# Optimization experiments

Measured on AMD Instinct MI355X. Metric: run time of the kernel, lower is better.

The kernel has to match this reference:

```python
import jax, jax.numpy as jnp
import numpy as np
from jax import lax

N_CLASS = 21
K_ED = 5
ALPHA = 0.1
BN_EPS = 1e-5


def _conv(x, w):
    # NCHW conv, stride 1, SAME padding
    return lax.conv_general_dilated(x, w, (1, 1), 'SAME',
                                    dimension_numbers=('NCHW', 'OIHW', 'NCHW'))


def _bn(x, g, b, m, v):
    # inference-mode BatchNorm2d with running stats
    scale = (g * lax.rsqrt(v + BN_EPS))[None, :, None, None]
    return (x - m[None, :, None, None]) * scale + b[None, :, None, None]


def _maxpool(x, k):
    return lax.reduce_window(x, -jnp.inf, lax.max, (1, 1, k, k), (1, 1, 1, 1), 'SAME')


def setup_inputs() -> dict:
    key = jax.random.key(0)
    ks = jax.random.split(key, 12)
    N, F, H, W, C = 8, 512, 96, 96, N_CLASS
    feature = jax.random.normal(ks[0], (N, F, H, W), jnp.float32)
    global_pred = jax.random.normal(ks[1], (N, C, H, W), jnp.float32)
    conv1_w = jax.random.normal(ks[2], (256, F, 3, 3), jnp.float32) * 0.02
    bn1_g = jnp.ones((256,), jnp.float32)
    bn1_b = jnp.zeros((256,), jnp.float32)
    bn1_m = jax.random.normal(ks[3], (256,), jnp.float32) * 0.1
    bn1_v = jax.random.uniform(ks[4], (256,), jnp.float32, 0.5, 1.5)
    conv2_w = jax.random.normal(ks[5], (128, 256, 3, 3), jnp.float32) * 0.02
    bn2_g = jnp.ones((128,), jnp.float32)
    bn2_b = jnp.zeros((128,), jnp.float32)
    bn2_m = jax.random.normal(ks[6], (128,), jnp.float32) * 0.1
    bn2_v = jax.random.uniform(ks[7], (128,), jnp.float32, 0.5, 1.5)
    conv3_w = jax.random.normal(ks[8], (C, 128, 1, 1), jnp.float32) * 0.02
    conv3_b = jnp.zeros((C,), jnp.float32)
    return dict(feature=feature, global_pred=global_pred,
                conv1_w=conv1_w, bn1_g=bn1_g, bn1_b=bn1_b, bn1_m=bn1_m, bn1_v=bn1_v,
                conv2_w=conv2_w, bn2_g=bn2_g, bn2_b=bn2_b, bn2_m=bn2_m, bn2_v=bn2_v,
                conv3_w=conv3_w, conv3_b=conv3_b)


def reference(feature, global_pred, conv1_w, bn1_g, bn1_b, bn1_m, bn1_v,
              conv2_w, bn2_g, bn2_b, bn2_m, bn2_v, conv3_w, conv3_b):
    N, F, H, W = feature.shape
    # hard labels -> one-hot [N, C, H, W]
    lbl = jnp.argmax(global_pred, axis=1)
    onehot = jnp.transpose(jax.nn.one_hot(lbl, N_CLASS, dtype=feature.dtype), (0, 3, 1, 2))
    # binary morphology: dilation = max-pool, erosion = -max-pool(-x)
    d = _maxpool(onehot, K_ED)
    e = -_maxpool(-onehot, K_ED)
    transition = jnp.sum(d - e, axis=1, keepdims=True)
    transition = jnp.where(transition >= 1.0, 1.0, transition)  # [N,1,H,W]
    tfeat = feature * transition
    # per-class masked mean over ALL H*W pixels (faithful to .mean(dim=2))
    objs = jnp.einsum('nfhw,nchw->ncf', feature, e) / (H * W)  # [N,C,F]
    # cdist(p=2) between transition-feature pixels and class prototypes
    x = tfeat.reshape(N, F, H * W).transpose(0, 2, 1)  # [N,HW,F]
    x2 = jnp.sum(x * x, axis=-1, keepdims=True)
    o2 = jnp.sum(objs * objs, axis=-1)
    d2 = jnp.maximum(x2 + o2[:, None, :] - 2.0 * jnp.einsum('npf,ncf->npc', x, objs), 0.0)
    cd = jnp.where(d2 > 0, jnp.sqrt(jnp.where(d2 > 0, d2, 1.0)), 0.0)  # safe sqrt
    dist = 1.0 - jax.nn.softmax(cd, axis=-1)  # [N,HW,C]
    obj_feat = jnp.einsum('npc,ncf->nfp', dist, objs).reshape(N, F, H, W)
    fusion = (feature * (1.0 - transition)
              + feature * transition * ALPHA
              + obj_feat * transition * (1.0 - ALPHA))
    # fusion_predictor: convBNReLU -> bilinear x2 -> convBNReLU -> 1x1 conv
    h = jax.nn.relu(_bn(_conv(fusion, conv1_w), bn1_g, bn1_b, bn1_m, bn1_v))
    h = jax.image.resize(h, (N, 256, 2 * H, 2 * W), method='bilinear')
    h = jax.nn.relu(_bn(_conv(h, conv2_w), bn2_g, bn2_b, bn2_m, bn2_v))
    logits = _conv(h, conv3_w) + conv3_b[None, :, None, None]
    # eval mode: softmax over classes
    return jax.nn.softmax(logits, axis=1)
```

## Files before the change

kernel.cpp:

```cpp
#include <hip/hip_runtime.h>
#include <cstdint>
#include <cstddef>

typedef __attribute__((ext_vector_type(4))) float f32x4;
typedef __attribute__((ext_vector_type(8))) short short8;

__device__ __forceinline__ float bf2f(unsigned short u) {
  union { unsigned int i; float f; } x; x.i = ((unsigned int)u) << 16; return x.f;
}
__device__ __forceinline__ unsigned short f2bf(float f) {
  union { float f; unsigned int i; } x; x.f = f;
  unsigned int r = x.i + 0x7fffu + ((x.i >> 16) & 1u);
  return (unsigned short)(r >> 16);
}
__device__ __forceinline__ void gload16(unsigned short* lds, const unsigned short* g) {
  __builtin_amdgcn_global_load_lds(
      (const __attribute__((address_space(1))) unsigned int*)g,
      (__attribute__((address_space(3))) unsigned int*)lds, 16, 0, 0);
}

__global__ void k_prepbn(const float* __restrict__ g1, const float* __restrict__ b1,
                         const float* __restrict__ m1, const float* __restrict__ v1,
                         const float* __restrict__ g2, const float* __restrict__ b2,
                         const float* __restrict__ m2, const float* __restrict__ v2,
                         float* __restrict__ s1, float* __restrict__ bb1,
                         float* __restrict__ s2, float* __restrict__ bb2) {
  int i = threadIdx.x;
  if (i < 256) { float s = g1[i] * rsqrtf(v1[i] + 1e-5f); s1[i] = s; bb1[i] = b1[i] - m1[i] * s; }
  if (i < 128) { float s = g2[i] * rsqrtf(v2[i] + 1e-5f); s2[i] = s; bb2[i] = b2[i] - m2[i] * s; }
}

__global__ void k_prepw1(const float* __restrict__ w, unsigned short* __restrict__ wt) {
  int i = blockIdx.x * 256 + threadIdx.x;
  int o = i / 4608, k = i - o * 4608;
  int cblk = k / 288, r = k - cblk * 288;
  int t = r >> 5, cl = r & 31;
  int ci = cblk * 32 + cl;
  int ty = t / 3, tx = t - ty * 3;
  wt[i] = f2bf(w[((o * 512 + ci) * 3 + ty) * 3 + tx]);
}
__global__ void k_prepw2(const float* __restrict__ w, unsigned short* __restrict__ wt) {
  int i = blockIdx.x * 256 + threadIdx.x;
  int o = i / 2304, k = i - o * 2304;
  int cblk = k / 288, r = k - cblk * 288;
  int t = r >> 5, cl = r & 31;
  int ci = cblk * 32 + cl;
  int ty = t / 3, tx = t - ty * 3;
  wt[i] = f2bf(w[((o * 256 + ci) * 3 + ty) * 3 + tx]);
}
__global__ void k_prepw3(const float* __restrict__ w3, unsigned short* __restrict__ w3b) {
  int i = blockIdx.x * 256 + threadIdx.x;
  int c = i >> 7, k = i & 127;
  w3b[i] = (c < 21) ? f2bf(w3[c * 128 + k]) : (unsigned short)0;
}

template <int HP, int WP, int C>
__global__ void k_border(unsigned short* __restrict__ p) {
  const int B = 2 * WP + 2 * (HP - 2);
  const int total = 8 * B * (C / 8);
  int i = blockIdx.x * 256 + threadIdx.x;
  if (i >= total) return;
  const int cg = i % (C / 8);
  int b = i / (C / 8);
  const int n = b / B; b -= n * B;
  int y, x;
  if (b < WP) { y = 0; x = b; }
  else if (b < 2 * WP) { y = HP - 1; x = b - WP; }
  else { int r = b - 2 * WP; y = 1 + (r >> 1); x = (r & 1) ? (WP - 1) : 0; }
  short8 z = {0, 0, 0, 0, 0, 0, 0, 0};
  *(short8*)&p[(((long)n * HP + y) * WP + x) * C + cg * 8] = z;
}

__global__ __launch_bounds__(256)
void k_featT(const float* __restrict__ feat, unsigned short* __restrict__ featT) {
  const int g = blockIdx.x * 256 + threadIdx.x;
  const int n = g / 9216, p = g - n * 9216;
  const int fg0 = blockIdx.y * 16;
  const float* src = feat + (long)n * 512 * 9216 + p;
  unsigned short* dst = featT + ((long)n * 9216 + p) * 512;
  for (int fg = fg0; fg < fg0 + 16; fg++) {
    short8 o;
    #pragma unroll
    for (int j = 0; j < 8; j++) o[j] = (short)f2bf(src[(long)(fg * 8 + j) * 9216]);
    *(short8*)&dst[fg * 8] = o;
  }
}

__global__ void k_labels(const float* __restrict__ gp, signed char* __restrict__ lab) {
  int p = blockIdx.x * 256 + threadIdx.x;
  int n = p / 9216, q = p - n * 9216;
  const float* g = gp + (long)n * 21 * 9216 + q;
  float best = g[0]; int bi = 0;
  #pragma unroll
  for (int c = 1; c < 21; c++) {
    float v = g[(long)c * 9216];
    if (v > best) { best = v; bi = c; }
  }
  lab[p] = (signed char)bi;
}

__global__ void k_em(const signed char* __restrict__ lab, signed char* __restrict__ em) {
  int p = blockIdx.x * 256 + threadIdx.x;
  int n = p / 9216, q = p - n * 9216, y = q / 96, x = q - y * 96;
  const signed char* L = lab + n * 9216;
  signed char l0 = L[q];
  bool uni = true;
  for (int dy = -2; dy <= 2; dy++) {
    int yy = y + dy; if (yy < 0 || yy > 95) continue;
    for (int dx = -2; dx <= 2; dx++) {
      int xx = x + dx; if (xx < 0 || xx > 95) continue;
      uni = uni && (L[yy * 96 + xx] == l0);
    }
  }
  em[p] = uni ? l0 : (signed char)-1;
}

__global__ __launch_bounds__(256)
void k_objsT(const unsigned short* __restrict__ featT, const signed char* __restrict__ em,
             float* __restrict__ objs) {
  __shared__ float part[21 * 512];
  __shared__ signed char emL[256];
  __shared__ int pres[21];
  const int b = blockIdx.x;
  const int n = b / 36;
  const int px0 = (b - n * 36) * 256;
  const int tid = threadIdx.x;
  for (int i = tid; i < 21 * 512; i += 256) part[i] = 0.f;
  if (tid < 21) pres[tid] = 0;
  emL[tid] = em[n * 9216 + px0 + tid];
  __syncthreads();
  const unsigned short* base = featT + ((long)n * 9216 + px0) * 512 + tid * 2;
  for (int px = 0; px < 256; px++) {
    const int c0 = emL[px];
    if (c0 >= 0) {
      if (tid == 0) pres[c0] = 1;
      unsigned int v = *(const unsigned int*)&base[(long)px * 512];
      atomicAdd(&part[c0 * 512 + tid * 2], bf2f((unsigned short)(v & 0xffff)));
      atomicAdd(&part[c0 * 512 + tid * 2 + 1], bf2f((unsigned short)(v >> 16)));
    }
  }
  __syncthreads();
  for (int i = tid; i < 21 * 512; i += 256) {
    const int c = i >> 9;
    if (pres[c]) atomicAdd(&objs[(long)n * 21 * 512 + i], part[i] * (1.0f / 9216.0f));
  }
}

__global__ void k_o2(const float* __restrict__ objs, float* __restrict__ o2) {
  int nc = blockIdx.x;
  int lane = threadIdx.x;
  const float* o = objs + (long)nc * 512;
  float s = 0.f;
  for (int f = lane; f < 512; f += 64) { float v = o[f]; s += v * v; }
  #pragma unroll
  for (int off = 32; off; off >>= 1) s += __shfl_down(s, off);
  if (lane == 0) o2[nc] = s;
}

__global__ void k_objsbf(const float* __restrict__ objs, unsigned short* __restrict__ oc) {
  int i = blockIdx.x * 256 + threadIdx.x;
  int n = i / (32 * 512); int r = i - n * 32 * 512;
  int c = r >> 9, f = r & 511;
  oc[i] = (c < 21) ? f2bf(objs[((long)n * 21 + c) * 512 + f]) : (unsigned short)0;
}

__global__ __launch_bounds__(256)
void k_dist_mfma(const unsigned short* __restrict__ featT,
                 const unsigned short* __restrict__ objs_c,
                 const float* __restrict__ o2, float* __restrict__ dist) {
  const int n = blockIdx.y;
  const int w = threadIdx.x >> 6, lane = threadIdx.x & 63;
  const int lrow = lane & 15, kg = lane >> 4;
  const int px = blockIdx.x * 64 + w * 16 + lrow;
  const unsigned short* fb = featT + ((long)n * 9216 + px) * 512 + kg * 8;
  const unsigned short* a0p = objs_c + ((long)n * 32 + lrow) * 512 + kg * 8;
  const unsigned short* a1p = a0p + 16 * 512;
  f32x4 acc0 = {0.f, 0.f, 0.f, 0.f}, acc1 = {0.f, 0.f, 0.f, 0.f};
  float x2 = 0.f;
  #pragma unroll
  for (int s = 0; s < 16; s++) {
    const short8 b = *(const short8*)&fb[s * 32];
    const short8 a0 = *(const short8*)&a0p[s * 32];
    const short8 a1 = *(const short8*)&a1p[s * 32];
    acc0 = __builtin_amdgcn_mfma_f32_16x16x32_bf16(a0, b, acc0, 0, 0, 0);
    acc1 = __builtin_amdgcn_mfma_f32_16x16x32_bf16(a1, b, acc1, 0, 0, 0);
    #pragma unroll
    for (int j = 0; j < 8; j++) { float v = bf2f((unsigned short)b[j]); x2 += v * v; }
  }
  x2 += __shfl_xor(x2, 16); x2 += __shfl_xor(x2, 32);
  float cd[8], mx = -1e30f;
  #pragma unroll
  for (int r = 0; r < 4; r++) {
    const int c = kg * 4 + r;
    float d2 = x2 + o2[n * 21 + c] - 2.f * acc0[r];
    cd[r] = sqrtf(fmaxf(d2, 0.f)); mx = fmaxf(mx, cd[r]);
  }
  #pragma unroll
  for (int r = 0; r < 4; r++) {
    const int c = 16 + kg * 4 + r;
    if (c < 21) {
      float d2 = x2 + o2[n * 21 + c] - 2.f * acc1[r];
      cd[4 + r] = sqrtf(fmaxf(d2, 0.f)); mx = fmaxf(mx, cd[4 + r]);
    } else cd[4 + r] = -1e30f;
  }
  mx = fmaxf(mx, __shfl_xor(mx, 16)); mx = fmaxf(mx, __shfl_xor(mx, 32));
  float sum = 0.f;
  #pragma unroll
  for (int k = 0; k < 8; k++) {
    cd[k] = (cd[k] > -1e29f) ? __expf(cd[k] - mx) : 0.f;
    sum += cd[k];
  }
  sum += __shfl_xor(sum, 16); sum += __shfl_xor(sum, 32);
  const float inv = 1.f / sum;
  #pragma unroll
  for (int r = 0; r < 4; r++)
    dist[((long)n * 21 + kg * 4 + r) * 9216 + px] = 1.f - cd[r] * inv;
  #pragma unroll
  for (int r = 0; r < 4; r++) {
    const int c = 16 + kg * 4 + r;
    if (c < 21) dist[((long)n * 21 + c) * 9216 + px] = 1.f - cd[4 + r] * inv;
  }
}

__global__ __launch_bounds__(256)
void k_fusion(const unsigned short* __restrict__ featT, const signed char* __restrict__ em,
              const float* __restrict__ dist, const float* __restrict__ objs,
              unsigned short* __restrict__ fuP) {
  __shared__ float ob[21 * 512];
  __shared__ float dl[64][21];
  __shared__ signed char eml[64];
  const int blk = blockIdx.x;
  const int n = blk / 144;
  const int p0 = (blk - n * 144) * 64;
  const int tid = threadIdx.x;
  for (int i = tid; i < 21 * 512; i += 256) ob[i] = objs[(long)n * 21 * 512 + i];
  for (int i = tid; i < 64 * 21; i += 256) {
    int px = i & 63, c = i >> 6;
    dl[px][c] = dist[((long)n * 21 + c) * 9216 + p0 + px];
  }
  if (tid < 64) eml[tid] = em[n * 9216 + p0 + tid];
  __syncthreads();
  const int px = tid & 63;
  const int fg = (tid >> 6) * 8;
  const int q = p0 + px;
  const int y = q / 96, x = q - y * 96;
  unsigned short* dst = fuP + (((long)n * 98 + y + 1) * 98 + (x + 1)) * 512;
  const bool t = eml[px] < 0;
  const unsigned short* srcT = featT + ((long)n * 9216 + q) * 512;
  for (int f0 = 0; f0 < 512; f0 += 32) {
    short8 o;
    const short8 fvv = *(const short8*)&srcT[f0 + fg];
    #pragma unroll
    for (int j = 0; j < 8; j++) {
      const int f = f0 + fg + j;
      float fv = bf2f((unsigned short)fvv[j]);
      if (t) {
        float of = 0.f;
        #pragma unroll
        for (int c = 0; c < 21; c++) of += dl[px][c] * ob[c * 512 + f];
        fv = 0.1f * fv + 0.9f * of;
      }
      o[j] = (short)f2bf(fv);
    }
    *(short8*)&dst[fg] = o;
    dst += 32;
  }
}

template <int CIN, int NK>
__global__ __launch_bounds__(256)
void conv3x3_gemm(const unsigned short* __restrict__ inP,
                  const unsigned short* __restrict__ wT,
                  const float* __restrict__ scale, const float* __restrict__ bias,
                  unsigned short* __restrict__ out,
                  int Hout, int Wout, int Hp, int Wp, int COUT, int nbN) {
  __shared__ unsigned short ldsA[4][4096];
  __shared__ unsigned short ldsB[4][4096];
  const int tid = threadIdx.x;
  const int chunk = gridDim.x >> 3;
  const int bid = (blockIdx.x & 7) * chunk + (blockIdx.x >> 3);
  const int mb = bid / nbN, nb = bid - mb * nbN;
  const int bm0 = mb * 128, bn0 = nb * 128;
  const int KT = 9 * CIN;
  const int HWo = Hout * Wout;

  const int rA = tid >> 2;
  const int ch8 = (((tid & 3) ^ ((tid >> 3) & 3)) * 8);
  const int m0 = bm0 + rA, m1 = m0 + 64;
  const int n0 = m0 / HWo; const int q0 = m0 - n0 * HWo;
  const int y0 = q0 / Wout, x0 = q0 - y0 * Wout;
  const int n1 = m1 / HWo; const int q1 = m1 - n1 * HWo;
  const int y1 = q1 / Wout, x1 = q1 - y1 * Wout;
  const unsigned short* gA0 = inP + ((long)(n0 * Hp + y0) * Wp + x0) * CIN + ch8;
  const unsigned short* gA1 = inP + ((long)(n1 * Hp + y1) * Wp + x1) * CIN + ch8;
  const unsigned short* gB0 = wT + (long)(bn0 + rA) * KT + ch8;
  const unsigned short* gB1 = wT + (long)(bn0 + rA + 64) * KT + ch8;

  const int lane = tid & 63;
  const int wv = tid >> 6;
  const int wr = wv >> 1, wc = wv & 1;
  const int lrow = lane & 15, kg = lane >> 4;
  const int arow = wr * 64 + lrow;
  const int aoff = arow * 32 + (kg ^ ((arow >> 1) & 3)) * 8;
  const int brow = wc * 64 + lrow;
  const int boff = brow * 32 + (kg ^ ((brow >> 1) & 3)) * 8;

  f32x4 acc[4][4];
  const f32x4 zero = {0.f, 0.f, 0.f, 0.f};
  #pragma unroll
  for (int i = 0; i < 4; i++)
    #pragma unroll
    for (int j = 0; j < 4; j++) acc[i][j] = zero;

  auto stage = [&](int b, int s) {
    const int cblk = s / 9;
    const int t = s - cblk * 9;
    const int ty = t / 3, tx = t - ty * 3;
    const long offA = (long)(ty * Wp + tx) * CIN + cblk * 32;
    gload16(&ldsA[b][tid * 8], gA0 + offA);
    gload16(&ldsA[b][2048 + tid * 8], gA1 + offA);
    const long k0 = (long)s * 32;
    gload16(&ldsB[b][tid * 8], gB0 + k0);
    gload16(&ldsB[b][2048 + tid * 8], gB1 + k0);
  };

  auto kstep = [&](int rd) {
    const unsigned short* A = ldsA[rd];
    const unsigned short* B = ldsB[rd];
    short8 af[4], bfr[4];
    #pragma unroll
    for (int i = 0; i < 4; i++) af[i] = *(const short8*)&A[aoff + i * 512];
    #pragma unroll
    for (int j = 0; j < 4; j++) bfr[j] = *(const short8*)&B[boff + j * 512];
    __builtin_amdgcn_s_setprio(1);
    #pragma unroll
    for (int i = 0; i < 4; i++)
      #pragma unroll
      for (int j = 0; j < 4; j++)
        acc[i][j] = __builtin_amdgcn_mfma_f32_16x16x32_bf16(af[i], bfr[j], acc[i][j], 0, 0, 0);
    __builtin_amdgcn_s_setprio(0);
  };

  stage(0, 0);
  stage(1, 1);
  stage(2, 2);
  for (int s = 0; s < NK; ++s) {
    if (s <= NK - 3)
      asm volatile("s_waitcnt vmcnt(8)" ::: "memory");
    else if (s == NK - 2)
      asm volatile("s_waitcnt vmcnt(4)" ::: "memory");
    else
      asm volatile("s_waitcnt vmcnt(0)" ::: "memory");
    __builtin_amdgcn_s_barrier();
    asm volatile("" ::: "memory");
    kstep(s & 3);
    if (s + 3 < NK) stage((s + 3) & 3, s + 3);
  }

  #pragma unroll
  for (int i = 0; i < 4; i++) {
    const int row = bm0 + wr * 64 + i * 16 + kg * 4;
    #pragma unroll
    for (int j = 0; j < 4; j++) {
      const int col = bn0 + wc * 64 + j * 16 + lrow;
      const float sc = scale[col], bi = bias[col];
      #pragma unroll
      for (int r = 0; r < 4; r++) {
        float v = acc[i][j][r] * sc + bi;
        v = v > 0.f ? v : 0.f;
        out[(long)(row + r) * COUT + col] = f2bf(v);
      }
    }
  }
}

__global__ __launch_bounds__(256)
void conv2_fused(const unsigned short* __restrict__ inP,
                 const unsigned short* __restrict__ wT,
                 const float* __restrict__ scale, const float* __restrict__ bias,
                 const unsigned short* __restrict__ w3b, const float* __restrict__ b3,
                 float* __restrict__ out) {
  constexpr int CIN = 256, NK = 72;
  constexpr int Wout = 192, Hp = 194, Wp = 194;
  constexpr int HWo = 192 * 192;
  constexpr int KT = 9 * CIN;
  __shared__ unsigned short pool[6 * 4096];
  const int tid = threadIdx.x;
  const int chunk = gridDim.x >> 3;
  const int bid = (blockIdx.x & 7) * chunk + (blockIdx.x >> 3);
  const int bm0 = bid * 128;

  const int rA = tid >> 2;
  const int ch8 = (((tid & 3) ^ ((tid >> 3) & 3)) * 8);
  const int m0 = bm0 + rA, m1 = m0 + 64;
  const int n0 = m0 / HWo; const int q0 = m0 - n0 * HWo;
  const int y0 = q0 / Wout, x0 = q0 - y0 * Wout;
  const int n1 = m1 / HWo; const int q1 = m1 - n1 * HWo;
  const int y1 = q1 / Wout, x1 = q1 - y1 * Wout;
  const unsigned short* gA0 = inP + ((long)(n0 * Hp + y0) * Wp + x0) * CIN + ch8;
  const unsigned short* gA1 = inP + ((long)(n1 * Hp + y1) * Wp + x1) * CIN + ch8;
  const unsigned short* gB0 = wT + (long)rA * KT + ch8;
  const unsigned short* gB1 = wT + (long)(rA + 64) * KT + ch8;

  const int lane = tid & 63;
  const int wv = tid >> 6;
  const int wr = wv >> 1, wc = wv & 1;
  const int lrow = lane & 15, kg = lane >> 4;
  const int arow = wr * 64 + lrow;
  const int aoff = arow * 32 + (kg ^ ((arow >> 1) & 3)) * 8;
  const int brow = wc * 64 + lrow;
  const int boff = brow * 32 + (kg ^ ((brow >> 1) & 3)) * 8;

  f32x4 acc[4][4];
  const f32x4 zero = {0.f, 0.f, 0.f, 0.f};
  #pragma unroll
  for (int i = 0; i < 4; i++)
    #pragma unroll
    for (int j = 0; j < 4; j++) acc[i][j] = zero;

  auto stage = [&](int b, int s) {
    const int cblk = s / 9;
    const int t = s - cblk * 9;
    const int ty = t / 3, tx = t - ty * 3;
    const long offA = (long)(ty * Wp + tx) * CIN + cblk * 32;
    gload16(&pool[b * 4096 + tid * 8], gA0 + offA);
    gload16(&pool[b * 4096 + 2048 + tid * 8], gA1 + offA);
    const long k0 = (long)s * 32;
    gload16(&pool[12288 + b * 4096 + tid * 8], gB0 + k0);
    gload16(&pool[12288 + b * 4096 + 2048 + tid * 8], gB1 + k0);
  };

  auto kstep = [&](int rd) {
    const unsigned short* A = &pool[rd * 4096];
    const unsigned short* B = &pool[12288 + rd * 4096];
    short8 af[4], bfr[4];
    #pragma unroll
    for (int i = 0; i < 4; i++) af[i] = *(const short8*)&A[aoff + i * 512];
    #pragma unroll
    for (int j = 0; j < 4; j++) bfr[j] = *(const short8*)&B[boff + j * 512];
    __builtin_amdgcn_s_setprio(1);
    #pragma unroll
    for (int i = 0; i < 4; i++)
      #pragma unroll
      for (int j = 0; j < 4; j++)
        acc[i][j] = __builtin_amdgcn_mfma_f32_16x16x32_bf16(af[i], bfr[j], acc[i][j], 0, 0, 0);
    __builtin_amdgcn_s_setprio(0);
  };

  stage(0, 0);
  stage(1, 1);
  int rd = 0;
  for (int s = 0; s < NK; ++s) {
    if (s < NK - 1)
      asm volatile("s_waitcnt vmcnt(4)" ::: "memory");
    else
      asm volatile("s_waitcnt vmcnt(0)" ::: "memory");
    __builtin_amdgcn_s_barrier();
    asm volatile("" ::: "memory");
    kstep(rd);
    if (s + 2 < NK) stage((rd + 2 >= 3) ? rd - 1 : rd + 2, s + 2);
    rd = (rd == 2) ? 0 : rd + 1;
  }

  asm volatile("s_waitcnt lgkmcnt(0)" ::: "memory");
  __builtin_amdgcn_s_barrier();
  asm volatile("" ::: "memory");
  #pragma unroll
  for (int j = 0; j < 4; j++) {
    const int ch = wc * 64 + j * 16 + lrow;
    const float sc = scale[ch], bi = bias[ch];
    #pragma unroll
    for (int i = 0; i < 4; i++) {
      const int pxb = wr * 64 + i * 16 + kg * 4;
      #pragma unroll
      for (int r = 0; r < 4; r++) {
        const int px = pxb + r;
        float v = acc[i][j][r] * sc + bi;
        v = v > 0.f ? v : 0.f;
        pool[px * 128 + (ch ^ ((px & 7) << 3))] = f2bf(v);
      }
    }
  }
  asm volatile("s_waitcnt lgkmcnt(0)" ::: "memory");
  __builtin_amdgcn_s_barrier();
  asm volatile("" ::: "memory");

  #pragma unroll
  for (int g = 0; g < 2; g++) {
    const int px = wv * 32 + g * 16 + lrow;
    f32x4 acc0 = {0.f, 0.f, 0.f, 0.f}, acc1 = {0.f, 0.f, 0.f, 0.f};
    #pragma unroll
    for (int s = 0; s < 4; s++) {
      const int ch0 = s * 32 + kg * 8;
      const short8 b = *(const short8*)&pool[px * 128 + (ch0 ^ ((px & 7) << 3))];
      const short8 a0 = *(const short8*)&w3b[lrow * 128 + ch0];
      const short8 a1 = *(const short8*)&w3b[(16 + lrow) * 128 + ch0];
      acc0 = __builtin_amdgcn_mfma_f32_16x16x32_bf16(a0, b, acc0, 0, 0, 0);
      acc1 = __builtin_amdgcn_mfma_f32_16x16x32_bf16(a1, b, acc1, 0, 0, 0);
    }
    float lg[8], mx = -1e30f;
    #pragma unroll
    for (int r = 0; r < 4; r++) {
      lg[r] = acc0[r] + b3[kg * 4 + r];
      mx = fmaxf(mx, lg[r]);
    }
    #pragma unroll
    for (int r = 0; r < 4; r++) {
      const int c = 16 + kg * 4 + r;
      if (c < 21) { lg[4 + r] = acc1[r] + b3[c]; mx = fmaxf(mx, lg[4 + r]); }
      else lg[4 + r] = -1e30f;
    }
    mx = fmaxf(mx, __shfl_xor(mx, 16)); mx = fmaxf(mx, __shfl_xor(mx, 32));
    float sum = 0.f;
    #pragma unroll
    for (int k = 0; k < 8; k++) {
      lg[k] = (lg[k] > -1e29f) ? __expf(lg[k] - mx) : 0.f;
      sum += lg[k];
    }
    sum += __shfl_xor(sum, 16); sum += __shfl_xor(sum, 32);
    const float inv = 1.f / sum;
    const int m = bm0 + px;
    const int n = m / HWo;
    const int q = m - n * HWo;
    #pragma unroll
    for (int r = 0; r < 4; r++)
      out[((long)n * 21 + kg * 4 + r) * (long)HWo + q] = lg[r] * inv;
    #pragma unroll
    for (int r = 0; r < 4; r++) {
      const int c = 16 + kg * 4 + r;
      if (c < 21) out[((long)n * 21 + c) * (long)HWo + q] = lg[4 + r] * inv;
    }
  }
}

__global__ void k_upsample(const unsigned short* __restrict__ h1,
                           unsigned short* __restrict__ h2P) {
  const int idx = blockIdx.x * 256 + threadIdx.x;
  const int c8 = (idx & 31) * 8;
  const int p = idx >> 5;
  const int n = p / 36864; const int rr = p - n * 36864;
  const int Y = rr / 192, X = rr - Y * 192;
  const int ky = Y >> 1, kx = X >> 1;
  int yA, yB, xA, xB; float wyA, wyB, wxA, wxB;
  if ((Y & 1) == 0) { yA = ky > 0 ? ky - 1 : 0; yB = ky; wyA = 0.25f; wyB = 0.75f; }
  else { yA = ky; yB = ky < 95 ? ky + 1 : 95; wyA = 0.75f; wyB = 0.25f; }
  if ((X & 1) == 0) { xA = kx > 0 ? kx - 1 : 0; xB = kx; wxA = 0.25f; wxB = 0.75f; }
  else { xA = kx; xB = kx < 95 ? kx + 1 : 95; wxA = 0.75f; wxB = 0.25f; }
  const unsigned short* hb = h1 + (long)n * 96 * 96 * 256 + c8;
  const short8 vaa = *(const short8*)&hb[((long)yA * 96 + xA) * 256];
  const short8 vab = *(const short8*)&hb[((long)yA * 96 + xB) * 256];
  const short8 vba = *(const short8*)&hb[((long)yB * 96 + xA) * 256];
  const short8 vbb = *(const short8*)&hb[((long)yB * 96 + xB) * 256];
  short8 o;
  #pragma unroll
  for (int j = 0; j < 8; j++) {
    float v = wyA * (wxA * bf2f((unsigned short)vaa[j]) + wxB * bf2f((unsigned short)vab[j])) +
              wyB * (wxA * bf2f((unsigned short)vba[j]) + wxB * bf2f((unsigned short)vbb[j]));
    o[j] = (short)f2bf(v);
  }
  *(short8*)&h2P[(((long)n * 194 + Y + 1) * 194 + X + 1) * 256 + c8] = o;
}

extern "C" void kernel_launch(void* const* d_in, const int* in_sizes, int n_in,
                              void* d_out, int out_size, void* d_ws, size_t ws_size,
                              hipStream_t stream) {
  const float* feature = (const float*)d_in[0];
  const float* gp = (const float*)d_in[1];
  const float* w1 = (const float*)d_in[2];
  const float* g1 = (const float*)d_in[3];
  const float* b1 = (const float*)d_in[4];
  const float* m1 = (const float*)d_in[5];
  const float* v1 = (const float*)d_in[6];
  const float* w2 = (const float*)d_in[7];
  const float* g2 = (const float*)d_in[8];
  const float* b2 = (const float*)d_in[9];
  const float* m2 = (const float*)d_in[10];
  const float* v2 = (const float*)d_in[11];
  const float* w3 = (const float*)d_in[12];
  const float* b3 = (const float*)d_in[13];
  float* out = (float*)d_out;

  char* ws = (char*)d_ws;
  size_t off = 0;
  auto alloc = [&](size_t bytes) -> void* {
    void* p = ws + off;
    off += (bytes + 255) & ~(size_t)255;
    return p;
  };
  signed char* lab = (signed char*)alloc(73728);
  signed char* em = (signed char*)alloc(73728);
  float* objs = (float*)alloc(8 * 21 * 512 * 4);
  float* o2 = (float*)alloc(168 * 4);
  unsigned short* objs_c = (unsigned short*)alloc((size_t)8 * 32 * 512 * 2);
  float* dist = (float*)alloc((size_t)8 * 21 * 9216 * 4);
  unsigned short* w1t = (unsigned short*)alloc((size_t)256 * 4608 * 2);
  unsigned short* w2t = (unsigned short*)alloc((size_t)128 * 2304 * 2);
  unsigned short* w3b = (unsigned short*)alloc((size_t)32 * 128 * 2);
  float* s1 = (float*)alloc(256 * 4);
  float* bb1 = (float*)alloc(256 * 4);
  float* s2 = (float*)alloc(128 * 4);
  float* bb2 = (float*)alloc(128 * 4);
  const size_t fuP_bytes = (size_t)8 * 98 * 98 * 512 * 2;
  unsigned short* fuP = (unsigned short*)alloc(fuP_bytes);
  const size_t h1_bytes = (size_t)8 * 96 * 96 * 256 * 2;
  unsigned short* h1 = (unsigned short*)alloc(h1_bytes);
  const size_t h2P_bytes = (size_t)8 * 194 * 194 * 256 * 2;
  unsigned short* h2P = (unsigned short*)alloc(h2P_bytes);
  unsigned short* featT = h2P;

  if (off > ws_size) return;

  k_prepbn<<<1, 256, 0, stream>>>(g1, b1, m1, v1, g2, b2, m2, v2, s1, bb1, s2, bb2);
  k_prepw1<<<4608, 256, 0, stream>>>(w1, w1t);
  k_prepw2<<<1152, 256, 0, stream>>>(w2, w2t);
  k_prepw3<<<16, 256, 0, stream>>>(w3, w3b);

  k_border<98, 98, 512><<<777, 256, 0, stream>>>(fuP);
  hipMemsetAsync(objs, 0, 8 * 21 * 512 * 4, stream);

  k_labels<<<288, 256, 0, stream>>>(gp, lab);
  k_em<<<288, 256, 0, stream>>>(lab, em);
  k_featT<<<dim3(288, 4), 256, 0, stream>>>(feature, featT);
  k_objsT<<<288, 256, 0, stream>>>(featT, em, objs);
  k_o2<<<168, 64, 0, stream>>>(objs, o2);
  k_objsbf<<<512, 256, 0, stream>>>(objs, objs_c);
  k_dist_mfma<<<dim3(144, 8), 256, 0, stream>>>(featT, objs_c, o2, dist);
  k_fusion<<<1152, 256, 0, stream>>>(featT, em, dist, objs, fuP);

  conv3x3_gemm<512, 144><<<1152, 256, 0, stream>>>(fuP, w1t, s1, bb1, h1,
                                                   96, 96, 98, 98, 256, 2);
  k_border<194, 194, 256><<<772, 256, 0, stream>>>(h2P);
  k_upsample<<<36864, 256, 0, stream>>>(h1, h2P);
  conv2_fused<<<2304, 256, 0, stream>>>(h2P, w2t, s2, bb2, w3b, b3, out);
}
```

Baseline: 800.5 us.

## Shrink conv3x3 GEMM pipeline to 3 LDS stages and fuse objs finalize kernels

The conv3x3 implicit-GEMM kernel goes from a 4-buffer LDS ring to 3 buffers. Each iteration now issues the next stage load after a barrier and then waits with vmcnt before the compute step. This cuts LDS use from 64KB to 48KB per block, which could allow more resident blocks, but adds a second barrier per k-step and gives less prefetch depth. Separately, the o2 norm and bf16 conversion of the class prototypes are merged into one small kernel, saving a launch.

```diff
diff --git a/kernel.cpp b/kernel.cpp
--- a/kernel.cpp
+++ b/kernel.cpp
@@ -146,22 +146,26 @@
   }
 }
 
-__global__ void k_o2(const float* __restrict__ objs, float* __restrict__ o2) {
-  int nc = blockIdx.x;
-  int lane = threadIdx.x;
-  const float* o = objs + (long)nc * 512;
-  float s = 0.f;
-  for (int f = lane; f < 512; f += 64) { float v = o[f]; s += v * v; }
-  #pragma unroll
-  for (int off = 32; off; off >>= 1) s += __shfl_down(s, off);
-  if (lane == 0) o2[nc] = s;
-}
-
-__global__ void k_objsbf(const float* __restrict__ objs, unsigned short* __restrict__ oc) {
-  int i = blockIdx.x * 256 + threadIdx.x;
-  int n = i / (32 * 512); int r = i - n * 32 * 512;
-  int c = r >> 9, f = r & 511;
-  oc[i] = (c < 21) ? f2bf(objs[((long)n * 21 + c) * 512 + f]) : (unsigned short)0;
+__global__ void k_objfin(const float* __restrict__ objs, float* __restrict__ o2,
+                         unsigned short* __restrict__ oc) {
+  const int b = blockIdx.x;
+  const int n = b >> 5, c = b & 31;
+  const int lane = threadIdx.x;
+  unsigned short* dst = oc + ((long)n * 32 + c) * 512;
+  if (c < 21) {
+    const float* o = objs + ((long)n * 21 + c) * 512;
+    float s = 0.f;
+    for (int f = lane; f < 512; f += 64) {
+      float v = o[f];
+      s += v * v;
+      dst[f] = f2bf(v);
+    }
+    #pragma unroll
+    for (int off = 32; off; off >>= 1) s += __shfl_down(s, off);
+    if (lane == 0) o2[n * 21 + c] = s;
+  } else {
+    for (int f = lane; f < 512; f += 64) dst[f] = 0;
+  }
 }
 
 __global__ __launch_bounds__(256)
@@ -274,8 +278,8 @@
                   const float* __restrict__ scale, const float* __restrict__ bias,
                   unsigned short* __restrict__ out,
                   int Hout, int Wout, int Hp, int Wp, int COUT, int nbN) {
-  __shared__ unsigned short ldsA[4][4096];
-  __shared__ unsigned short ldsB[4][4096];
+  __shared__ unsigned short ldsA[3][4096];
+  __shared__ unsigned short ldsB[3][4096];
   const int tid = threadIdx.x;
   const int chunk = gridDim.x >> 3;
   const int bid = (blockIdx.x & 7) * chunk + (blockIdx.x >> 3);
@@ -343,19 +347,26 @@
 
   stage(0, 0);
   stage(1, 1);
-  stage(2, 2);
-  for (int s = 0; s < NK; ++s) {
-    if (s <= NK - 3)
-      asm volatile("s_waitcnt vmcnt(8)" ::: "memory");
-    else if (s == NK - 2)
-      asm volatile("s_waitcnt vmcnt(4)" ::: "memory");
-    else
-      asm volatile("s_waitcnt vmcnt(0)" ::: "memory");
+  int rd = 0, prev = 2;
+  for (int s = 0; s < NK - 2; ++s) {
     __builtin_amdgcn_s_barrier();
     asm volatile("" ::: "memory");
-    kstep(s & 3);
-    if (s + 3 < NK) stage((s + 3) & 3, s + 3);
-  }
+    stage(prev, s + 2);
+    asm volatile("s_waitcnt vmcnt(8)" ::: "memory");
+    __builtin_amdgcn_s_barrier();
+    asm volatile("" ::: "memory");
+    kstep(rd);
+    prev = rd; rd = (rd == 2) ? 0 : rd + 1;
+  }
+  asm volatile("s_waitcnt vmcnt(4)" ::: "memory");
+  __builtin_amdgcn_s_barrier();
+  asm volatile("" ::: "memory");
+  kstep(rd);
+  rd = (rd == 2) ? 0 : rd + 1;
+  asm volatile("s_waitcnt vmcnt(0)" ::: "memory");
+  __builtin_amdgcn_s_barrier();
+  asm volatile("" ::: "memory");
+  kstep(rd);
 
   #pragma unroll
   for (int i = 0; i < 4; i++) {
@@ -622,8 +633,7 @@
   k_em<<<288, 256, 0, stream>>>(lab, em);
   k_featT<<<dim3(288, 4), 256, 0, stream>>>(feature, featT);
   k_objsT<<<288, 256, 0, stream>>>(featT, em, objs);
-  k_o2<<<168, 64, 0, stream>>>(objs, o2);
-  k_objsbf<<<512, 256, 0, stream>>>(objs, objs_c);
+  k_objfin<<<256, 64, 0, stream>>>(objs, o2, objs_c);
   k_dist_mfma<<<dim3(144, 8), 256, 0, stream>>>(featT, objs_c, o2, dist);
   k_fusion<<<1152, 256, 0, stream>>>(featT, em, dist, objs, fuP);
 
```

Result: faster. 765.3 us (-4.4%).
